# Kernel tuning notes

Hardware: AMD Instinct MI355X
Metric: run time of the kernel (lower is better)

Reference implementation:

```python
import jax, jax.numpy as jnp
import numpy as np

B, T, K = 256, 512, 128


def setup_inputs() -> dict:
    key = jax.random.key(0)
    k1, k2, k3, k4 = jax.random.split(key, 4)
    logits = jax.random.normal(k1, (B, T, K), dtype=jnp.float32)
    labels = jax.random.randint(k2, (B, T), 0, K, dtype=jnp.int32)
    seq_lens = jax.random.randint(k3, (B,), 1, T + 1, dtype=jnp.int32)
    trans = jax.random.uniform(k4, (K, K), dtype=jnp.float32)
    return {"logits": logits, "labels": labels, "seq_lens": seq_lens, "trans": trans}


def _crf_neg_log_likelihood(logits, labels, seq_lens, trans):
    # logits: [B,T,K], labels: [B,T] int, seq_lens: [B] int, trans: [K,K]
    Bb, Tt, Kk = logits.shape
    mask = (jnp.arange(Tt)[None, :] < seq_lens[:, None])  # [B,T] bool

    # ---- gold sequence score ----
    unary = jnp.take_along_axis(logits, labels[..., None].astype(jnp.int32), axis=-1)[..., 0]  # [B,T]
    unary_score = jnp.sum(jnp.where(mask, unary, 0.0), axis=-1)  # [B]
    pair = trans[labels[:, :-1], labels[:, 1:]]  # [B,T-1]
    pair_score = jnp.sum(jnp.where(mask[:, 1:], pair, 0.0), axis=-1)  # [B]
    score = unary_score + pair_score  # [B]

    # ---- log partition via forward algorithm (lax.scan over time) ----
    alpha0 = logits[:, 0]  # [B,K]
    xs = (jnp.swapaxes(logits[:, 1:], 0, 1), jnp.swapaxes(mask[:, 1:], 0, 1))  # [T-1,B,K],[T-1,B]

    def step(alpha, x):
        logit_t, m_t = x
        # alpha[:, :, None] + trans[None] : [B, K_prev, K_next]
        new = jax.nn.logsumexp(alpha[:, :, None] + trans[None, :, :], axis=1) + logit_t
        alpha = jnp.where(m_t[:, None], new, alpha)
        return alpha, None

    alpha, _ = jax.lax.scan(step, alpha0, xs)
    log_z = jax.nn.logsumexp(alpha, axis=-1)  # [B]

    log_likelihood = score - log_z
    return jnp.sum(-log_likelihood)  # scalar, matches tf.reduce_sum(-ll)


def reference(logits, labels, seq_lens, trans):
    return _crf_neg_log_likelihood(logits, labels, seq_lens, trans)
```

## Files before the change

kernel.cpp:

```cpp
#include <hip/hip_runtime.h>

#define Bdim 256
#define Tdim 512
#define Kdim 128
#define NT   512

#define BAR() asm volatile("s_waitcnt lgkmcnt(0)\n\ts_barrier" ::: "memory")

template <int CTRL>
__device__ __forceinline__ float quad_add(float v) {
    int r = __builtin_amdgcn_update_dpp(0, __float_as_int(v), CTRL, 0xF, 0xF, true);
    return v + __int_as_float(r);
}

__global__ __launch_bounds__(NT, 1) void crf_nll_kernel(
    const float* __restrict__ logits,
    const int*   __restrict__ labels,
    const int*   __restrict__ seq_lens,
    const float* __restrict__ trans,
    float* __restrict__ out)
{
    const int b   = blockIdx.x;
    const int tid = threadIdx.x;
    const int j   = tid >> 2;
    const int g   = tid & 3;
    const int L   = seq_lens[b];

    __shared__ float pbuf[2][Kdim];
    __shared__ float sred[NT / 64];
    __shared__ float ared[NT / 64];

    const int*   lab_b   = labels + (size_t)b * Tdim;
    const float* logit_b = logits + (size_t)b * Tdim * Kdim;

    float e[32];
    #pragma unroll
    for (int u = 0; u < 8; ++u) {
        const int row0 = g * 32 + (((u + g) & 7) << 2);
        #pragma unroll
        for (int c = 0; c < 4; ++c)
            e[u * 4 + c] = __expf(trans[(row0 + c) * Kdim + j]);
    }

    float s = 0.f;
    {
        const int t = tid;
        if (t < L) {
            const int lb = lab_b[t];
            s = logit_b[(size_t)t * Kdim + lb];
            if (t >= 1) s += trans[lab_b[t - 1] * Kdim + lb];
        }
    }
    #pragma unroll
    for (int o = 32; o > 0; o >>= 1) s += __shfl_down(s, o, 64);
    if ((tid & 63) == 0) sred[tid >> 6] = s;

    float a = 0.f, off = 0.f;
    if (g == 0) {
        a = __expf(logit_b[j]);
        pbuf[0][j] = a;
    }
    int cb = 0;
    __syncthreads();

    float score = 0.f;
    if (tid == 0) {
        #pragma unroll
        for (int w = 0; w < NT / 64; ++w) score += sred[w];
    }

    float curl[8], nxtl[8];
    #pragma unroll
    for (int u = 0; u < 8; ++u) {
        const int tt = 1 + u;
        curl[u] = (tt < Tdim) ? logit_b[(size_t)tt * Kdim + j] : 0.f;
    }

    for (int tb = 1; tb < L; tb += 8) {
        #pragma unroll
        for (int u = 0; u < 8; ++u) {
            const int tt = tb + 8 + u;
            nxtl[u] = (tt < Tdim) ? logit_b[(size_t)tt * Kdim + j] : 0.f;
        }
        #pragma unroll
        for (int u = 0; u < 8; ++u) {
            const int t = tb + u;
            if (t < L) {
                const float4* p4 = (const float4*)pbuf[cb];
                float p0 = 1.f;
                float acc0 = 0.f, acc1 = 0.f, acc2 = 0.f, acc3 = 0.f;
                #pragma unroll
                for (int uu = 0; uu < 8; ++uu) {
                    const int idx = (g << 3) + ((uu + g) & 7);
                    const float4 p = p4[idx];
                    if (uu == 0) {
                        if (g == 0) p0 = p.x;
                    }
                    acc0 = fmaf(p.x, e[uu * 4 + 0], acc0);
                    acc1 = fmaf(p.y, e[uu * 4 + 1], acc1);
                    acc2 = fmaf(p.z, e[uu * 4 + 2], acc2);
                    acc3 = fmaf(p.w, e[uu * 4 + 3], acc3);
                }
                const float lp0 = __logf(p0);
                float acc = (acc0 + acc1) + (acc2 + acc3);
                acc = quad_add<0xB1>(acc);
                acc = quad_add<0x4E>(acc);
                if (g == 0) {
                    a = acc * __expf(curl[u] - lp0);
                    off += lp0;
                    pbuf[cb ^ 1][j] = a;
                }
                cb ^= 1;
                BAR();
            }
        }
        #pragma unroll
        for (int u = 0; u < 8; ++u) curl[u] = nxtl[u];
    }

    float as = (g == 0) ? a : 0.f;
    #pragma unroll
    for (int o = 32; o > 0; o >>= 1) as += __shfl_down(as, o, 64);
    if ((tid & 63) == 0) ared[tid >> 6] = as;
    __syncthreads();
    if (tid == 0) {
        float tot = 0.f;
        #pragma unroll
        for (int w = 0; w < NT / 64; ++w) tot += ared[w];
        const float logz = off + __logf(tot);
        atomicAdd(out, logz - score);
    }
}

extern "C" void kernel_launch(void* const* d_in, const int* in_sizes, int n_in,
                              void* d_out, int out_size, void* d_ws, size_t ws_size,
                              hipStream_t stream) {
    const float* logits   = (const float*)d_in[0];
    const int*   labels   = (const int*)d_in[1];
    const int*   seq_lens = (const int*)d_in[2];
    const float* trans    = (const float*)d_in[3];
    float* out = (float*)d_out;

    (void)hipMemsetAsync(out, 0, sizeof(float), stream);
    crf_nll_kernel<<<dim3(Bdim), dim3(NT), 0, stream>>>(
        logits, labels, seq_lens, trans, out);
}
```

Baseline: 268.8 us.

## Halve block size and register-tile 4x4 transition outer products per thread

Result: slower. 274.7 us (+2.2%).

```diff
diff --git a/kernel.cpp b/kernel.cpp
--- a/kernel.cpp
+++ b/kernel.cpp
@@ -3,7 +3,7 @@
 #define Bdim 256
 #define Tdim 512
 #define Kdim 128
-#define NT   512
+#define NT   256
 
 #define BAR() asm volatile("s_waitcnt lgkmcnt(0)\n\ts_barrier" ::: "memory")
 
@@ -22,8 +22,9 @@
 {
     const int b   = blockIdx.x;
     const int tid = threadIdx.x;
-    const int j   = tid >> 2;
-    const int g   = tid & 3;
+    const int j4  = tid >> 3;
+    const int g   = tid & 7;
+    const int cj  = 4 * j4 + (g & 3);
     const int L   = seq_lens[b];
 
     __shared__ float pbuf[2][Kdim];
@@ -33,21 +34,28 @@
     const int*   lab_b   = labels + (size_t)b * Tdim;
     const float* logit_b = logits + (size_t)b * Tdim * Kdim;
 
-    float e[32];
+    float e[4][4][4];
     #pragma unroll
-    for (int u = 0; u < 8; ++u) {
-        const int row0 = g * 32 + (((u + g) & 7) << 2);
+    for (int ii4 = 0; ii4 < 4; ++ii4) {
+        const int row0 = 16 * g + (((ii4 + g) & 3) << 2);
         #pragma unroll
-        for (int c = 0; c < 4; ++c)
-            e[u * 4 + c] = __expf(trans[(row0 + c) * Kdim + j]);
+        for (int ci = 0; ci < 4; ++ci) {
+            const float4 tr =
+                *(const float4*)&trans[(size_t)(row0 + ci) * Kdim + 4 * j4];
+            e[ii4][ci][0] = __expf(tr.x);
+            e[ii4][ci][1] = __expf(tr.y);
+            e[ii4][ci][2] = __expf(tr.z);
+            e[ii4][ci][3] = __expf(tr.w);
+        }
     }
 
     float s = 0.f;
-    {
-        const int t = tid;
+    #pragma unroll
+    for (int t0 = 0; t0 < Tdim; t0 += NT) {
+        const int t = t0 + tid;
         if (t < L) {
             const int lb = lab_b[t];
-            s = logit_b[(size_t)t * Kdim + lb];
+            s += logit_b[(size_t)t * Kdim + lb];
             if (t >= 1) s += trans[lab_b[t - 1] * Kdim + lb];
         }
     }
@@ -56,9 +64,9 @@
     if ((tid & 63) == 0) sred[tid >> 6] = s;
 
     float a = 0.f, off = 0.f;
-    if (g == 0) {
-        a = __expf(logit_b[j]);
-        pbuf[0][j] = a;
+    if (g < 4) {
+        a = __expf(logit_b[cj]);
+        pbuf[0][cj] = a;
     }
     int cb = 0;
     __syncthreads();
@@ -73,42 +81,58 @@
     #pragma unroll
     for (int u = 0; u < 8; ++u) {
         const int tt = 1 + u;
-        curl[u] = (tt < Tdim) ? logit_b[(size_t)tt * Kdim + j] : 0.f;
+        curl[u] = (tt < Tdim) ? logit_b[(size_t)tt * Kdim + cj] : 0.f;
     }
 
     for (int tb = 1; tb < L; tb += 8) {
         #pragma unroll
         for (int u = 0; u < 8; ++u) {
             const int tt = tb + 8 + u;
-            nxtl[u] = (tt < Tdim) ? logit_b[(size_t)tt * Kdim + j] : 0.f;
+            nxtl[u] = (tt < Tdim) ? logit_b[(size_t)tt * Kdim + cj] : 0.f;
         }
         #pragma unroll
         for (int u = 0; u < 8; ++u) {
             const int t = tb + u;
             if (t < L) {
                 const float4* p4 = (const float4*)pbuf[cb];
-                float p0 = 1.f;
+                const float p0 = pbuf[cb][0];
+                const float lp0 = __logf(p0);
+                const float sc  = __expf(curl[u] - lp0);
                 float acc0 = 0.f, acc1 = 0.f, acc2 = 0.f, acc3 = 0.f;
                 #pragma unroll
-                for (int uu = 0; uu < 8; ++uu) {
-                    const int idx = (g << 3) + ((uu + g) & 7);
-                    const float4 p = p4[idx];
-                    if (uu == 0) {
-                        if (g == 0) p0 = p.x;
-                    }
-                    acc0 = fmaf(p.x, e[uu * 4 + 0], acc0);
-                    acc1 = fmaf(p.y, e[uu * 4 + 1], acc1);
-                    acc2 = fmaf(p.z, e[uu * 4 + 2], acc2);
-                    acc3 = fmaf(p.w, e[uu * 4 + 3], acc3);
+                for (int ii4 = 0; ii4 < 4; ++ii4) {
+                    const float4 p = p4[(g << 2) + ((ii4 + g) & 3)];
+                    acc0 = fmaf(p.x, e[ii4][0][0], acc0);
+                    acc1 = fmaf(p.x, e[ii4][0][1], acc1);
+                    acc2 = fmaf(p.x, e[ii4][0][2], acc2);
+                    acc3 = fmaf(p.x, e[ii4][0][3], acc3);
+                    acc0 = fmaf(p.y, e[ii4][1][0], acc0);
+                    acc1 = fmaf(p.y, e[ii4][1][1], acc1);
+                    acc2 = fmaf(p.y, e[ii4][1][2], acc2);
+                    acc3 = fmaf(p.y, e[ii4][1][3], acc3);
+                    acc0 = fmaf(p.z, e[ii4][2][0], acc0);
+                    acc1 = fmaf(p.z, e[ii4][2][1], acc1);
+                    acc2 = fmaf(p.z, e[ii4][2][2], acc2);
+                    acc3 = fmaf(p.z, e[ii4][2][3], acc3);
+                    acc0 = fmaf(p.w, e[ii4][3][0], acc0);
+                    acc1 = fmaf(p.w, e[ii4][3][1], acc1);
+                    acc2 = fmaf(p.w, e[ii4][3][2], acc2);
+                    acc3 = fmaf(p.w, e[ii4][3][3], acc3);
                 }
-                const float lp0 = __logf(p0);
-                float acc = (acc0 + acc1) + (acc2 + acc3);
-                acc = quad_add<0xB1>(acc);
-                acc = quad_add<0x4E>(acc);
-                if (g == 0) {
-                    a = acc * __expf(curl[u] - lp0);
-                    off += lp0;
-                    pbuf[cb ^ 1][j] = a;
+                off += lp0;
+                acc0 = quad_add<0xB1>(acc0); acc0 = quad_add<0x4E>(acc0);
+                acc1 = quad_add<0xB1>(acc1); acc1 = quad_add<0x4E>(acc1);
+                acc2 = quad_add<0xB1>(acc2); acc2 = quad_add<0x4E>(acc2);
+                acc3 = quad_add<0xB1>(acc3); acc3 = quad_add<0x4E>(acc3);
+                float sel  = (g & 1) ? acc1 : acc0;
+                float selh = (g & 1) ? acc3 : acc2;
+                sel = (g & 2) ? selh : sel;
+                sel += __int_as_float(__builtin_amdgcn_ds_swizzle(
+                           __float_as_int(sel), 0x101F));
+                const float anew = sel * sc;
+                if (g < 4) {
+                    a = anew;
+                    pbuf[cb ^ 1][cj] = anew;
                 }
                 cb ^= 1;
                 BAR();
@@ -118,7 +142,7 @@
         for (int u = 0; u < 8; ++u) curl[u] = nxtl[u];
     }
 
-    float as = (g == 0) ? a : 0.f;
+    float as = (g < 4) ? a : 0.f;
     #pragma unroll
     for (int o = 32; o > 0; o >>= 1) as += __shfl_down(as, o, 64);
     if ((tid & 63) == 0) ared[tid >> 6] = as;
```
